# Kernel optimization log

Measured on AMD Instinct MI355X. Metric: run time of the kernel, lower is better.

The kernel has to match this reference:

```python
import jax, jax.numpy as jnp
import numpy as np

B, T, U = 4, 256, 64
D_ENC, D_DEC, V = 512, 512, 1024
IN_F = D_ENC + D_DEC  # 1024


def setup_inputs() -> dict:
    key = jax.random.key(0)
    ks = jax.random.split(key, 10)
    enc = jax.random.normal(ks[0], (B, T, D_ENC), dtype=jnp.float32)
    dec = jax.random.normal(ks[1], (B, U, D_DEC), dtype=jnp.float32)
    # ragged lengths in [len/2, len]; force max to be attained so padded
    # shape equals the torch packed output shape (MaxPad == (T, U)).
    enc_lens = jax.random.randint(ks[2], (B,), T // 2, T + 1, dtype=jnp.int32).at[0].set(T)
    dec_lens = jax.random.randint(ks[3], (B,), U // 2, U + 1, dtype=jnp.int32).at[0].set(U)
    s_e = 1.0 / np.sqrt(D_ENC)
    s_d = 1.0 / np.sqrt(D_DEC)
    s_f = 1.0 / np.sqrt(IN_F)
    W_enc = jax.random.uniform(ks[4], (D_ENC, IN_F), jnp.float32, -s_e, s_e)
    b_enc = jax.random.uniform(ks[5], (IN_F,), jnp.float32, -s_e, s_e)
    W_dec = jax.random.uniform(ks[6], (D_DEC, IN_F), jnp.float32, -s_d, s_d)
    b_dec = jax.random.uniform(ks[7], (IN_F,), jnp.float32, -s_d, s_d)
    W_fc = jax.random.uniform(ks[8], (IN_F, V), jnp.float32, -s_f, s_f)
    b_fc = jax.random.uniform(ks[9], (V,), jnp.float32, -s_f, s_f)
    return dict(enc=enc, dec=dec, W_enc=W_enc, b_enc=b_enc, W_dec=W_dec,
                b_dec=b_dec, W_fc=W_fc, b_fc=b_fc,
                enc_lens=enc_lens, dec_lens=dec_lens)


def reference(enc, dec, W_enc, b_enc, W_dec, b_dec, W_fc, b_fc, enc_lens, dec_lens):
    # per-frame / per-label projections: [B,T,IN_F], [B,U,IN_F]
    pe = jnp.einsum('btd,df->btf', enc, W_enc) + b_enc
    pd = jnp.einsum('bud,df->buf', dec, W_dec) + b_dec
    # broadcast-add joint grid: [B,T,U,IN_F]
    h = pe[:, :, None, :] + pd[:, None, :, :]
    logits = jnp.einsum('btuf,fv->btuv', jnp.tanh(h), W_fc) + b_fc
    logp = jax.nn.log_softmax(logits, axis=-1)
    # zero out cells beyond (enc_len_b, dec_len_b), matching F.pad(value=0.)
    t_ok = jnp.arange(T)[None, :] < enc_lens[:, None]          # [B,T]
    u_ok = jnp.arange(U)[None, :] < dec_lens[:, None]          # [B,U]
    mask = (t_ok[:, :, None] & u_ok[:, None, :])[..., None]    # [B,T,U,1]
    return jnp.where(mask, logp, 0.0)
```

## Files before the change

kernel.cpp:

```cpp
#include <hip/hip_runtime.h>
#include <hip/hip_bf16.h>


#define TT 256
#define UU 64
#define VV 1024
#define FF 1024
#define DK 512

typedef __bf16 bf16x8 __attribute__((ext_vector_type(8)));
typedef float  f32x16 __attribute__((ext_vector_type(16)));

__device__ __forceinline__ float fast_tanh(float x) {
  float ax = __builtin_fabsf(x);
  float e  = __expf(-2.0f * ax);
  float r  = (1.0f - e) * __builtin_amdgcn_rcpf(1.0f + e);
  return __builtin_copysignf(r, x);
}

__global__ __launch_bounds__(256)
void pack_w(const float* __restrict__ Wfc, const float* __restrict__ Wenc,
            const float* __restrict__ Wdec,
            __bf16* __restrict__ Pfc, __bf16* __restrict__ Pen, __bf16* __restrict__ Pde)
{
  int bi = blockIdx.x;
  const float* W; __bf16* P; int base;
  if (bi < 512)      { W = Wfc;  P = Pfc; base = bi; }
  else if (bi < 768) { W = Wenc; P = Pen; base = bi - 512; }
  else               { W = Wdec; P = Pde; base = bi - 768; }
  int idx = base * 256 + threadIdx.x;
  int k8 = idx >> 10, v = idx & 1023;
  bf16x8 o;
#pragma unroll
  for (int j = 0; j < 8; ++j) o[j] = (__bf16)W[(k8 * 8 + j) * 1024 + v];
  *(bf16x8*)(P + (size_t)idx * 8) = o;
}

__global__ __launch_bounds__(256)
void proj_mfma(const float* __restrict__ enc, const float* __restrict__ dec,
               const __bf16* __restrict__ Pen, const __bf16* __restrict__ Pde,
               const float* __restrict__ be, const float* __restrict__ bd,
               float* __restrict__ pe, float* __restrict__ pd)
{
  constexpr int BK = 128;
  __shared__ __align__(16) char As[2][64 * BK * 2];
  const int tid = threadIdx.x;
  const int lane = tid & 63;
  const int wid  = tid >> 6;
  const int l31  = lane & 31;
  const int lhi  = lane >> 5;

  int bi = blockIdx.x;
  const float* X; const __bf16* PW; const float* bias; float* P; int rt, ct;
  if (bi < 64) { X = enc; PW = Pen; bias = be; P = pe; rt = bi >> 2; ct = bi & 3; }
  else { int bj = bi - 64; X = dec; PW = Pde; bias = bd; P = pd; rt = bj >> 2; ct = bj & 3; }
  const int r0 = rt * 64;

  auto fillA = [&](int buf, int kc) {
#pragma unroll
    for (int i = 0; i < 4; ++i) {
      int tau = i * 256 + tid;
      int r = tau >> 4, g = tau & 15;
      int k = kc * BK + g * 8;
      const float4* x4 = (const float4*)(X + (r0 + r) * DK + k);
      float4 a0 = x4[0], a1 = x4[1];
      float xv[8] = {a0.x, a0.y, a0.z, a0.w, a1.x, a1.y, a1.z, a1.w};
      bf16x8 p;
#pragma unroll
      for (int q = 0; q < 8; ++q) p[q] = (__bf16)xv[q];
      *(bf16x8*)(&As[buf][r * (BK * 2) + ((g * 16) ^ ((r & 7) << 4))]) = p;
    }
  };

  f32x16 acc[2][2];
#pragma unroll
  for (int mi = 0; mi < 2; ++mi)
#pragma unroll
    for (int ni = 0; ni < 2; ++ni)
#pragma unroll
      for (int q = 0; q < 16; ++q) acc[mi][ni][q] = 0.f;

  fillA(0, 0);
  __syncthreads();
  const int colBase = ct * 256 + wid * 64 + l31;
  for (int kc = 0; kc < DK / BK; ++kc) {
    if (kc + 1 < DK / BK) fillA((kc + 1) & 1, kc + 1);
    const char* Ab = As[kc & 1];
#pragma unroll 2
    for (int ks = 0; ks < BK / 16; ++ks) {
      int k8 = (kc * 8 + ks) * 2 + lhi;
      bf16x8 bfr[2];
#pragma unroll
      for (int ni = 0; ni < 2; ++ni)
        bfr[ni] = *(const bf16x8*)(PW + ((size_t)k8 * VV + colBase + ni * 32) * 8);
      bf16x8 afr[2];
#pragma unroll
      for (int mi = 0; mi < 2; ++mi) {
        int ra = mi * 32 + l31;
        int kb = ks * 32 + lhi * 16;
        afr[mi] = *(const bf16x8*)(&Ab[ra * (BK * 2) + (kb ^ ((ra & 7) << 4))]);
      }
#pragma unroll
      for (int mi = 0; mi < 2; ++mi)
#pragma unroll
        for (int ni = 0; ni < 2; ++ni)
          acc[mi][ni] = __builtin_amdgcn_mfma_f32_32x32x16_bf16(afr[mi], bfr[ni], acc[mi][ni], 0, 0, 0);
    }
    __syncthreads();
  }
  float bv[2];
#pragma unroll
  for (int ni = 0; ni < 2; ++ni) bv[ni] = bias[colBase + ni * 32];
#pragma unroll
  for (int mi = 0; mi < 2; ++mi)
#pragma unroll
    for (int j = 0; j < 16; ++j) {
      int row = r0 + mi * 32 + (j & 3) + 8 * (j >> 2) + 4 * lhi;
#pragma unroll
      for (int ni = 0; ni < 2; ++ni)
        P[row * VV + colBase + ni * 32] = acc[mi][ni][j] + bv[ni];
    }
}

__global__ __launch_bounds__(512, 2)
void joint_main(const float* __restrict__ pe, const float* __restrict__ pd,
                const __bf16* __restrict__ pW, const float* __restrict__ bfc,
                const int* __restrict__ elens, const int* __restrict__ dlens,
                float* __restrict__ out)
{
  constexpr int BK = 128;
  __shared__ __align__(16) char As[2][64 * BK * 2];
  __shared__ float pr[8][64];
  __shared__ float lseS[64];

  const int blk = blockIdx.x;
  const int b = blk >> 8;
  const int t = blk & 255;
  const int tid = threadIdx.x;
  const int elen = elens[b], dlen = dlens[b];
  float* outBase = out + (size_t)blk * (UU * VV);

  if (t >= elen) {
    float4 z = {0.f, 0.f, 0.f, 0.f};
#pragma unroll 4
    for (int i = tid; i < UU * VV / 4; i += 512) ((float4*)outBase)[i] = z;
    return;
  }

  const int lane = tid & 63;
  const int wid  = tid >> 6;
  const int l31  = lane & 31;
  const int lhi  = lane >> 5;
  const int colLane = wid * 128 + l31;

  const float* peRow  = pe + (size_t)blk * FF;
  const float* pdBase = pd + (size_t)b * UU * FF;

  const int sr = tid >> 4;
  const int sg = tid & 15;

  float4 R[4];
  auto issueH = [&](int kc, int half) {
    int r = sr + half * 32;
    int k = kc * BK + sg * 8;
    const float4* e4 = (const float4*)(peRow + k);
    const float4* d4 = (const float4*)(pdBase + (size_t)r * FF + k);
    R[0] = e4[0]; R[1] = e4[1]; R[2] = d4[0]; R[3] = d4[1];
  };
  auto commitH = [&](int buf, int half) {
    int r = sr + half * 32;
    float hv[8] = {R[0].x + R[2].x, R[0].y + R[2].y, R[0].z + R[2].z, R[0].w + R[2].w,
                   R[1].x + R[3].x, R[1].y + R[3].y, R[1].z + R[3].z, R[1].w + R[3].w};
    bf16x8 p;
#pragma unroll
    for (int q = 0; q < 8; ++q) p[q] = (__bf16)fast_tanh(hv[q]);
    *(bf16x8*)(&As[buf][r * (BK * 2) + ((sg * 16) ^ ((r & 7) << 4))]) = p;
  };

  f32x16 acc[2][4];
#pragma unroll
  for (int mi = 0; mi < 2; ++mi)
#pragma unroll
    for (int ni = 0; ni < 4; ++ni)
#pragma unroll
      for (int q = 0; q < 16; ++q) acc[mi][ni][q] = 0.f;

  issueH(0, 0); commitH(0, 0);
  issueH(0, 1); commitH(0, 1);
  __syncthreads();

  auto mstep = [&](const char* Ab, int kc, int ks) {
    int k8 = (kc * 8 + ks) * 2 + lhi;
    bf16x8 bfr[4];
#pragma unroll
    for (int ni = 0; ni < 4; ++ni)
      bfr[ni] = *(const bf16x8*)(pW + ((size_t)k8 * VV + colLane + ni * 32) * 8);
    bf16x8 afr[2];
#pragma unroll
    for (int mi = 0; mi < 2; ++mi) {
      int ra = mi * 32 + l31;
      int kb = ks * 32 + lhi * 16;
      afr[mi] = *(const bf16x8*)(&Ab[ra * (BK * 2) + (kb ^ ((ra & 7) << 4))]);
    }
#pragma unroll
    for (int mi = 0; mi < 2; ++mi)
#pragma unroll
      for (int ni = 0; ni < 4; ++ni)
        acc[mi][ni] = __builtin_amdgcn_mfma_f32_32x32x16_bf16(afr[mi], bfr[ni], acc[mi][ni], 0, 0, 0);
  };

  for (int kc = 0; kc < FF / BK; ++kc) {
    const char* Ab = As[kc & 1];
    const int nb = (kc + 1) & 1;
    const bool more = (kc + 1) < FF / BK;
    if (more) issueH(kc + 1, 0);
#pragma unroll
    for (int ks = 0; ks < 4; ++ks) mstep(Ab, kc, ks);
    if (more) { commitH(nb, 0); issueH(kc + 1, 1); }
#pragma unroll
    for (int ks = 4; ks < 8; ++ks) mstep(Ab, kc, ks);
    if (more) commitH(nb, 1);
    __syncthreads();
  }

  float bias[4];
#pragma unroll
  for (int ni = 0; ni < 4; ++ni) bias[ni] = bfc[colLane + ni * 32];

  float rsum[2][16];
#pragma unroll
  for (int mi = 0; mi < 2; ++mi)
#pragma unroll
    for (int j = 0; j < 16; ++j) {
      float s = 0.f;
#pragma unroll
      for (int ni = 0; ni < 4; ++ni) {
        float v = acc[mi][ni][j] + bias[ni];
        acc[mi][ni][j] = v;
        s += __expf(v);
      }
      rsum[mi][j] = s;
    }
#pragma unroll
  for (int s = 1; s < 32; s <<= 1) {
#pragma unroll
    for (int mi = 0; mi < 2; ++mi)
#pragma unroll
      for (int j = 0; j < 16; ++j)
        rsum[mi][j] += __shfl_xor(rsum[mi][j], s, 64);
  }
#pragma unroll
  for (int mi = 0; mi < 2; ++mi)
#pragma unroll
    for (int j = 0; j < 16; ++j)
      if (l31 == j) {
        int row = mi * 32 + (j & 3) + 8 * (j >> 2) + 4 * lhi;
        pr[wid][row] = rsum[mi][j];
      }
  __syncthreads();
  if (tid < 64) {
    float s = 0.f;
#pragma unroll
    for (int w = 0; w < 8; ++w) s += pr[w][tid];
    lseS[tid] = __logf(s);
  }
  __syncthreads();

#pragma unroll
  for (int mi = 0; mi < 2; ++mi)
#pragma unroll
    for (int j = 0; j < 16; ++j) {
      int row = mi * 32 + (j & 3) + 8 * (j >> 2) + 4 * lhi;
      float l = lseS[row];
      bool valid = row < dlen;
#pragma unroll
      for (int ni = 0; ni < 4; ++ni) {
        float v = valid ? (acc[mi][ni][j] - l) : 0.0f;
        outBase[(size_t)row * VV + colLane + ni * 32] = v;
      }
    }
}

extern "C" void kernel_launch(void* const* d_in, const int* in_sizes, int n_in,
                              void* d_out, int out_size, void* d_ws, size_t ws_size,
                              hipStream_t stream)
{
  const float* enc  = (const float*)d_in[0];
  const float* dec  = (const float*)d_in[1];
  const float* Wenc = (const float*)d_in[2];
  const float* benc = (const float*)d_in[3];
  const float* Wdec = (const float*)d_in[4];
  const float* bdec = (const float*)d_in[5];
  const float* Wfc  = (const float*)d_in[6];
  const float* bfc  = (const float*)d_in[7];
  const int* elens  = (const int*)d_in[8];
  const int* dlens  = (const int*)d_in[9];
  float* out = (float*)d_out;

  float* pe = (float*)d_ws;
  float* pd = pe + 1024 * 1024;
  __bf16* Pfc = (__bf16*)(pd + 256 * 1024);
  __bf16* Pen = Pfc + 1024 * 1024;
  __bf16* Pde = Pen + 512 * 1024;

  pack_w<<<1024, 256, 0, stream>>>(Wfc, Wenc, Wdec, Pfc, Pen, Pde);
  proj_mfma<<<80, 256, 0, stream>>>(enc, dec, Pen, Pde, benc, bdec, pe, pd);
  joint_main<<<1024, 512, 0, stream>>>(pe, pd, Pfc, bfc, elens, dlens, out);
}
```

Measured before the change: 219.0 us.

## Double K-chunk size, remap block order, and use lighter LDS barrier

Raises the K tile from 128 to 256, so each thread computes twice as many tanh values per stage and the main loop runs half as many barrier-separated iterations. The LDS swizzle is widened to match the longer rows. Block indices are permuted across eight groups, which changes which (b,t) rows run together and may alter cache locality. The __syncthreads is replaced by an explicit lgkmcnt wait plus s_barrier with sched barriers. This doubles the LDS footprint and the register staging (R[8]), which could hurt occupancy at 2 blocks per CU.

```diff
diff --git a/kernel.cpp b/kernel.cpp
--- a/kernel.cpp
+++ b/kernel.cpp
@@ -16,6 +16,13 @@
   float e  = __expf(-2.0f * ax);
   float r  = (1.0f - e) * __builtin_amdgcn_rcpf(1.0f + e);
   return __builtin_copysignf(r, x);
+}
+
+__device__ __forceinline__ void kbarrier() {
+  asm volatile("s_waitcnt lgkmcnt(0)" ::: "memory");
+  __builtin_amdgcn_sched_barrier(0);
+  __builtin_amdgcn_s_barrier();
+  __builtin_amdgcn_sched_barrier(0);
 }
 
 __global__ __launch_bounds__(256)
@@ -128,12 +135,14 @@
                 const int* __restrict__ elens, const int* __restrict__ dlens,
                 float* __restrict__ out)
 {
-  constexpr int BK = 128;
-  __shared__ __align__(16) char As[2][64 * BK * 2];
+  constexpr int BK = 256;
+  constexpr int RB = BK * 2;
+  __shared__ __align__(16) char As[2][64 * RB];
   __shared__ float pr[8][64];
   __shared__ float lseS[64];
 
-  const int blk = blockIdx.x;
+  const int bid = blockIdx.x;
+  const int blk = (bid & 7) * 128 + (bid >> 3);
   const int b = blk >> 8;
   const int t = blk & 255;
   const int tid = threadIdx.x;
@@ -157,24 +166,32 @@
   const float* pdBase = pd + (size_t)b * UU * FF;
 
   const int sr = tid >> 4;
-  const int sg = tid & 15;
-
-  float4 R[4];
+  const int g0 = (tid & 15) * 2;
+
+  float4 R[8];
   auto issueH = [&](int kc, int half) {
-    int r = sr + half * 32;
-    int k = kc * BK + sg * 8;
+    int k = kc * BK + g0 * 8;
+    size_t ro = (size_t)(sr + half * 32) * FF;
     const float4* e4 = (const float4*)(peRow + k);
-    const float4* d4 = (const float4*)(pdBase + (size_t)r * FF + k);
+    const float4* d4 = (const float4*)(pdBase + ro + k);
     R[0] = e4[0]; R[1] = e4[1]; R[2] = d4[0]; R[3] = d4[1];
+    R[4] = e4[2]; R[5] = e4[3]; R[6] = d4[2]; R[7] = d4[3];
   };
   auto commitH = [&](int buf, int half) {
     int r = sr + half * 32;
-    float hv[8] = {R[0].x + R[2].x, R[0].y + R[2].y, R[0].z + R[2].z, R[0].w + R[2].w,
-                   R[1].x + R[3].x, R[1].y + R[3].y, R[1].z + R[3].z, R[1].w + R[3].w};
-    bf16x8 p;
-#pragma unroll
-    for (int q = 0; q < 8; ++q) p[q] = (__bf16)fast_tanh(hv[q]);
-    *(bf16x8*)(&As[buf][r * (BK * 2) + ((sg * 16) ^ ((r & 7) << 4))]) = p;
+    char* rowp = &As[buf][r * RB];
+    int sw = (r & 15) << 4;
+#pragma unroll
+    for (int q = 0; q < 2; ++q) {
+      float hv[8] = {R[4*q+0].x + R[4*q+2].x, R[4*q+0].y + R[4*q+2].y,
+                     R[4*q+0].z + R[4*q+2].z, R[4*q+0].w + R[4*q+2].w,
+                     R[4*q+1].x + R[4*q+3].x, R[4*q+1].y + R[4*q+3].y,
+                     R[4*q+1].z + R[4*q+3].z, R[4*q+1].w + R[4*q+3].w};
+      bf16x8 p;
+#pragma unroll
+      for (int e = 0; e < 8; ++e) p[e] = (__bf16)fast_tanh(hv[e]);
+      *(bf16x8*)(rowp + (((g0 + q) * 16) ^ sw)) = p;
+    }
   };
 
   f32x16 acc[2][4];
@@ -187,20 +204,20 @@
 
   issueH(0, 0); commitH(0, 0);
   issueH(0, 1); commitH(0, 1);
-  __syncthreads();
+  kbarrier();
 
   auto mstep = [&](const char* Ab, int kc, int ks) {
-    int k8 = (kc * 8 + ks) * 2 + lhi;
+    int k8 = (kc * 16 + ks) * 2 + lhi;
     bf16x8 bfr[4];
 #pragma unroll
     for (int ni = 0; ni < 4; ++ni)
       bfr[ni] = *(const bf16x8*)(pW + ((size_t)k8 * VV + colLane + ni * 32) * 8);
     bf16x8 afr[2];
+    int kb = ks * 32 + lhi * 16;
 #pragma unroll
     for (int mi = 0; mi < 2; ++mi) {
       int ra = mi * 32 + l31;
-      int kb = ks * 32 + lhi * 16;
-      afr[mi] = *(const bf16x8*)(&Ab[ra * (BK * 2) + (kb ^ ((ra & 7) << 4))]);
+      afr[mi] = *(const bf16x8*)(&Ab[ra * RB + (kb ^ ((ra & 15) << 4))]);
     }
 #pragma unroll
     for (int mi = 0; mi < 2; ++mi)
@@ -215,12 +232,12 @@
     const bool more = (kc + 1) < FF / BK;
     if (more) issueH(kc + 1, 0);
 #pragma unroll
-    for (int ks = 0; ks < 4; ++ks) mstep(Ab, kc, ks);
+    for (int ks = 0; ks < 8; ++ks) mstep(Ab, kc, ks);
     if (more) { commitH(nb, 0); issueH(kc + 1, 1); }
 #pragma unroll
-    for (int ks = 4; ks < 8; ++ks) mstep(Ab, kc, ks);
+    for (int ks = 8; ks < 16; ++ks) mstep(Ab, kc, ks);
     if (more) commitH(nb, 1);
-    __syncthreads();
+    kbarrier();
   }
 
   float bias[4];
```

After: 230.4 us. +5.2%, slower.

## Stage packed W_fc tiles into LDS via async global_load_lds double buffering

Applied to the files above, without the earlier changes.

The main joint GEMM previously read the packed bf16 W_fc fragments straight from global memory inside each MFMA step. It now copies each 32-row K-slice of W_fc (64KB) into a double-buffered LDS area using global_load_lds, and rebuilds the tanh(A) tile pipeline with a 64-wide K chunk and its own swizzle. Manual waitcnt, barriers and setprio schedule the copies to overlap with the MFMAs. The cost is about 144KB of LDS per block, which lowers occupancy below the declared 2 blocks per CU, and a barrier now runs on every 32-wide K step.

```diff
diff --git a/kernel.cpp b/kernel.cpp
--- a/kernel.cpp
+++ b/kernel.cpp
@@ -128,8 +128,8 @@
                 const int* __restrict__ elens, const int* __restrict__ dlens,
                 float* __restrict__ out)
 {
-  constexpr int BK = 128;
-  __shared__ __align__(16) char As[2][64 * BK * 2];
+  __shared__ __align__(16) unsigned char Bb[2][65536];
+  __shared__ __align__(16) unsigned char Ab[2][8192];
   __shared__ float pr[8][64];
   __shared__ float lseS[64];
 
@@ -156,25 +156,34 @@
   const float* peRow  = pe + (size_t)blk * FF;
   const float* pdBase = pd + (size_t)b * UU * FF;
 
-  const int sr = tid >> 4;
-  const int sg = tid & 15;
-
-  float4 R[4];
-  auto issueH = [&](int kc, int half) {
-    int r = sr + half * 32;
-    int k = kc * BK + sg * 8;
+  auto stageB = [&](int kc, int bi) {
+    const __bf16* gp0 = pW + (size_t)kc * 32768;
+#pragma unroll
+    for (int i = 0; i < 8; ++i) {
+      int fbase = i * 512 + wid * 64;
+      __builtin_amdgcn_global_load_lds(
+        (const __attribute__((address_space(1))) void*)(gp0 + ((size_t)(fbase + lane)) * 8),
+        (__attribute__((address_space(3))) void*)(&Bb[bi][fbase * 16]),
+        16, 0, 0);
+    }
+  };
+
+  float4 R0, R1, R2, R3;
+  const int ar = tid >> 3;
+  const int akg = tid & 7;
+  auto issueA = [&](int s) {
+    int k = s * 64 + akg * 8;
     const float4* e4 = (const float4*)(peRow + k);
-    const float4* d4 = (const float4*)(pdBase + (size_t)r * FF + k);
-    R[0] = e4[0]; R[1] = e4[1]; R[2] = d4[0]; R[3] = d4[1];
-  };
-  auto commitH = [&](int buf, int half) {
-    int r = sr + half * 32;
-    float hv[8] = {R[0].x + R[2].x, R[0].y + R[2].y, R[0].z + R[2].z, R[0].w + R[2].w,
-                   R[1].x + R[3].x, R[1].y + R[3].y, R[1].z + R[3].z, R[1].w + R[3].w};
+    const float4* d4 = (const float4*)(pdBase + (size_t)ar * FF + k);
+    R0 = e4[0]; R1 = e4[1]; R2 = d4[0]; R3 = d4[1];
+  };
+  auto commitA = [&](int s) {
+    float hv[8] = {R0.x + R2.x, R0.y + R2.y, R0.z + R2.z, R0.w + R2.w,
+                   R1.x + R3.x, R1.y + R3.y, R1.z + R3.z, R1.w + R3.w};
     bf16x8 p;
 #pragma unroll
-    for (int q = 0; q < 8; ++q) p[q] = (__bf16)fast_tanh(hv[q]);
-    *(bf16x8*)(&As[buf][r * (BK * 2) + ((sg * 16) ^ ((r & 7) << 4))]) = p;
+    for (int e = 0; e < 8; ++e) p[e] = (__bf16)fast_tanh(hv[e]);
+    *(bf16x8*)(&Ab[s & 1][ar * 128 + ((akg ^ (ar & 7)) << 4)]) = p;
   };
 
   f32x16 acc[2][4];
@@ -185,22 +194,18 @@
 #pragma unroll
       for (int q = 0; q < 16; ++q) acc[mi][ni][q] = 0.f;
 
-  issueH(0, 0); commitH(0, 0);
-  issueH(0, 1); commitH(0, 1);
-  __syncthreads();
-
-  auto mstep = [&](const char* Ab, int kc, int ks) {
-    int k8 = (kc * 8 + ks) * 2 + lhi;
+  auto mstep = [&](const unsigned char* Bbuf, const unsigned char* Abuf, int kc, int j) {
     bf16x8 bfr[4];
+    const int k8l = 2 * j + lhi;
 #pragma unroll
     for (int ni = 0; ni < 4; ++ni)
-      bfr[ni] = *(const bf16x8*)(pW + ((size_t)k8 * VV + colLane + ni * 32) * 8);
+      bfr[ni] = *(const bf16x8*)(Bbuf + ((size_t)((k8l << 10) + colLane + (ni << 5)) << 4));
     bf16x8 afr[2];
+    const int kg = ((kc & 1) << 2) + (j << 1) + lhi;
 #pragma unroll
     for (int mi = 0; mi < 2; ++mi) {
-      int ra = mi * 32 + l31;
-      int kb = ks * 32 + lhi * 16;
-      afr[mi] = *(const bf16x8*)(&Ab[ra * (BK * 2) + (kb ^ ((ra & 7) << 4))]);
+      int row = mi * 32 + l31;
+      afr[mi] = *(const bf16x8*)(Abuf + row * 128 + ((kg ^ (row & 7)) << 4));
     }
 #pragma unroll
     for (int mi = 0; mi < 2; ++mi)
@@ -209,18 +214,34 @@
         acc[mi][ni] = __builtin_amdgcn_mfma_f32_32x32x16_bf16(afr[mi], bfr[ni], acc[mi][ni], 0, 0, 0);
   };
 
-  for (int kc = 0; kc < FF / BK; ++kc) {
-    const char* Ab = As[kc & 1];
-    const int nb = (kc + 1) & 1;
-    const bool more = (kc + 1) < FF / BK;
-    if (more) issueH(kc + 1, 0);
-#pragma unroll
-    for (int ks = 0; ks < 4; ++ks) mstep(Ab, kc, ks);
-    if (more) { commitH(nb, 0); issueH(kc + 1, 1); }
-#pragma unroll
-    for (int ks = 4; ks < 8; ++ks) mstep(Ab, kc, ks);
-    if (more) commitH(nb, 1);
-    __syncthreads();
+  issueA(0);
+  commitA(0);
+  stageB(0, 0);
+  issueA(1);
+  asm volatile("s_waitcnt vmcnt(4)" ::: "memory");
+  asm volatile("s_waitcnt lgkmcnt(0)" ::: "memory");
+  __builtin_amdgcn_sched_barrier(0);
+  __builtin_amdgcn_s_barrier();
+  __builtin_amdgcn_sched_barrier(0);
+
+  for (int kc = 0; kc < 32; ++kc) {
+    if (kc < 31) stageB(kc + 1, (kc + 1) & 1);
+    if (kc >= 2 && (kc & 1) == 0 && (kc / 2 + 1) <= 15) issueA(kc / 2 + 1);
+    __builtin_amdgcn_sched_barrier(0);
+    const unsigned char* Bbuf = Bb[kc & 1];
+    const unsigned char* Abuf = Ab[(kc >> 1) & 1];
+    __builtin_amdgcn_s_setprio(1);
+    mstep(Bbuf, Abuf, kc, 0);
+    mstep(Bbuf, Abuf, kc, 1);
+    __builtin_amdgcn_s_setprio(0);
+    if ((kc & 1) == 1 && ((kc + 1) / 2) <= 15) commitA((kc + 1) / 2);
+    if (kc < 31) {
+      asm volatile("s_waitcnt vmcnt(0)" ::: "memory");
+      asm volatile("s_waitcnt lgkmcnt(0)" ::: "memory");
+      __builtin_amdgcn_sched_barrier(0);
+      __builtin_amdgcn_s_barrier();
+      __builtin_amdgcn_sched_barrier(0);
+    }
   }
 
   float bias[4];
```

After: 261.9 us. +19.6%, slower.
